# Kernel optimization log

Hardware: AMD Instinct MI355X
Metric: run time of the kernel (lower is better)

Reference implementation:

```python
import jax, jax.numpy as jnp
import numpy as np

T = 1024
H_DIM = 2048
VOCAB = 32000
N_EXPERTS = 8
TOP_K = 2
MOE_I = 1024
SHARED_I = 1024
N_HEADS = 16
Q_LORA = 512
KV_LORA = 256
NOPE = 64
ROPE = 32
V_D = 64
EPS = 1e-6
ROUTED_SCALE = 2.5
NEG = -1e30


def rmsnorm(x, w, eps=EPS):
    return x * jax.lax.rsqrt(jnp.mean(x * x, axis=-1, keepdims=True) + eps) * w


def rope_cos_sin(positions):
    inv_freq = 1.0 / (10000.0 ** (jnp.arange(0, ROPE, 2, dtype=jnp.float32) / ROPE))
    freqs = positions.astype(jnp.float32)[:, None] * inv_freq  # [T, ROPE//2]
    return jnp.cos(freqs), jnp.sin(freqs)


def apply_rope(x, cos, sin):
    # interleaved (non-neox) rotary, as DeepSeek MLA uses
    x1, x2 = x[..., 0::2], x[..., 1::2]
    return jnp.stack([x1 * cos - x2 * sin, x1 * sin + x2 * cos], axis=-1).reshape(x.shape)


def setup_inputs() -> dict:
    key = jax.random.key(0)
    ks = jax.random.split(key, 26)
    s = 0.02

    def w(k, shape, scale=s):
        return jax.random.normal(k, shape, dtype=jnp.float32) * scale

    return {
        'input_ids': jax.random.randint(ks[0], (T,), 0, VOCAB, dtype=jnp.int32),
        'positions': jnp.arange(T, dtype=jnp.int32),
        'previous_hidden_states': jax.random.normal(ks[1], (T, H_DIM), dtype=jnp.float32),
        'embed': w(ks[2], (VOCAB, H_DIM), 1.0),
        'enorm_w': jnp.ones((H_DIM,), jnp.float32),
        'hnorm_w': jnp.ones((H_DIM,), jnp.float32),
        'eh_proj_w': w(ks[3], (2 * H_DIM, H_DIM)),
        'in_ln_w': jnp.ones((H_DIM,), jnp.float32),
        'post_ln_w': jnp.ones((H_DIM,), jnp.float32),
        'q_a_w': w(ks[4], (H_DIM, Q_LORA)),
        'q_a_ln_w': jnp.ones((Q_LORA,), jnp.float32),
        'q_b_w': w(ks[5], (Q_LORA, N_HEADS * (NOPE + ROPE))),
        'kv_a_w': w(ks[6], (H_DIM, KV_LORA + ROPE)),
        'kv_a_ln_w': jnp.ones((KV_LORA,), jnp.float32),
        'kv_b_w': w(ks[7], (KV_LORA, N_HEADS * (NOPE + V_D))),
        'o_w': w(ks[8], (N_HEADS * V_D, H_DIM)),
        'gate_w': w(ks[9], (H_DIM, N_EXPERTS)),
        'gate_bias': w(ks[10], (N_EXPERTS,), 0.01),
        'expert_gate_w': w(ks[11], (N_EXPERTS, H_DIM, MOE_I)),
        'expert_up_w': w(ks[12], (N_EXPERTS, H_DIM, MOE_I)),
        'expert_down_w': w(ks[13], (N_EXPERTS, MOE_I, H_DIM)),
        'shared_gate_w': w(ks[14], (H_DIM, SHARED_I)),
        'shared_up_w': w(ks[15], (H_DIM, SHARED_I)),
        'shared_down_w': w(ks[16], (SHARED_I, H_DIM)),
    }


def reference(input_ids, positions, previous_hidden_states, embed, enorm_w, hnorm_w,
              eh_proj_w, in_ln_w, post_ln_w, q_a_w, q_a_ln_w, q_b_w, kv_a_w, kv_a_ln_w,
              kv_b_w, o_w, gate_w, gate_bias, expert_gate_w, expert_up_w, expert_down_w,
              shared_gate_w, shared_up_w, shared_down_w):
    # --- MTP head: RMSNorm x2 + concat + linear ---
    e = embed[input_ids]                                         # [T, h]
    cat_in = jnp.concatenate([rmsnorm(e, enorm_w),
                              rmsnorm(previous_hidden_states, hnorm_w)], axis=-1)
    x0 = cat_in @ eh_proj_w                                      # [T, h]

    # --- decoder layer: MLA attention ---
    resid = x0
    h = rmsnorm(x0, in_ln_w)
    q_a = rmsnorm(h @ q_a_w, q_a_ln_w)                           # [T, q_lora]
    q = (q_a @ q_b_w).reshape(T, N_HEADS, NOPE + ROPE)
    q_nope, q_pe = q[..., :NOPE], q[..., NOPE:]
    kv_a = h @ kv_a_w                                            # [T, kv_lora+rope]
    kv_c, k_pe = kv_a[:, :KV_LORA], kv_a[:, KV_LORA:]
    kv = (rmsnorm(kv_c, kv_a_ln_w) @ kv_b_w).reshape(T, N_HEADS, NOPE + V_D)
    k_nope, v = kv[..., :NOPE], kv[..., NOPE:]
    cos, sin = rope_cos_sin(positions)                           # [T, ROPE//2]
    q_pe = apply_rope(q_pe, cos[:, None, :], sin[:, None, :])
    k_pe = apply_rope(k_pe, cos, sin)
    qf = jnp.concatenate([q_nope, q_pe], axis=-1)                # [T, H, dq]
    kf = jnp.concatenate([k_nope,
                          jnp.broadcast_to(k_pe[:, None, :], (T, N_HEADS, ROPE))], axis=-1)
    scale = (NOPE + ROPE) ** -0.5
    scores = jnp.einsum('thd,shd->hts', qf, kf) * scale          # [H, T, T]
    causal = positions[:, None] >= positions[None, :]
    scores = jnp.where(causal[None], scores, NEG)
    probs = jax.nn.softmax(scores, axis=-1)
    o = jnp.einsum('hts,shv->thv', probs, v).reshape(T, N_HEADS * V_D)
    attn_out = o @ o_w

    resid = resid + attn_out
    h2 = rmsnorm(resid, post_ln_w)

    # --- DeepSeek-V3 MoE: sigmoid gating + bias-corrected top-k ---
    logits = h2 @ gate_w                                         # [T, E]
    sig = jax.nn.sigmoid(logits)
    _, top_idx = jax.lax.top_k(sig + gate_bias, TOP_K)           # selection uses bias
    top_w = jnp.take_along_axis(sig, top_idx, axis=1)            # weights from raw scores
    top_w = top_w / (jnp.sum(top_w, axis=-1, keepdims=True) + 1e-20)
    combine = (jax.nn.one_hot(top_idx, N_EXPERTS, dtype=h2.dtype)
               * top_w[..., None]).sum(axis=1) * ROUTED_SCALE    # [T, E]
    g = jnp.einsum('th,ehi->tei', h2, expert_gate_w)
    u = jnp.einsum('th,ehi->tei', h2, expert_up_w)
    d = jnp.einsum('tei,eih->teh', jax.nn.silu(g) * u, expert_down_w)
    routed = jnp.einsum('teh,te->th', d, combine)
    shared = (jax.nn.silu(h2 @ shared_gate_w) * (h2 @ shared_up_w)) @ shared_down_w
    mlp_out = routed + shared

    # module returns mtp_hidden + mtp_residual
    return mlp_out + resid
```

## Files before the change

### kernel.cpp

```cpp
#include <hip/hip_runtime.h>
#include <hip/hip_bf16.h>
#include <math.h>

constexpr int T_ = 1024;
constexpr int HDIM = 2048;
constexpr int NH = 16;
constexpr int QKD = 96;
constexpr int VD = 64;
constexpr int MAXTILES = 32;
constexpr float EPSF = 1e-6f;

using f32x4 = __attribute__((ext_vector_type(4))) float;
using s16x8 = __attribute__((ext_vector_type(8))) short;
using s16x4 = __attribute__((ext_vector_type(4))) short;

constexpr size_t OF_CATH  = 0;
constexpr size_t OF_CATL  = 2097152;
constexpr size_t OF_X0    = 4194304;
constexpr size_t OF_MACT  = 6291456;
constexpr size_t OF_HH    = 8388608;
constexpr size_t OF_HL    = 9437184;
constexpr size_t OF_QBUF  = 11010048;
constexpr size_t OF_KVBUF = 12877824;
constexpr size_t OF_QAH   = 14974976;
constexpr size_t OF_QAL   = 15237120;
constexpr size_t OF_KVCNH = 15499264;
constexpr size_t OF_KVCNL = 15630336;
constexpr size_t OF_QFH   = 15761408;
constexpr size_t OF_QFL   = 16547840;
constexpr size_t OF_KFH   = 17334272;
constexpr size_t OF_KFL   = 18120704;
constexpr size_t OF_VBH   = 18907136;
constexpr size_t OF_VBL   = 19431424;
constexpr size_t OF_OBH   = 19955712;
constexpr size_t OF_OBL   = 20480000;
constexpr size_t OF_ATT   = 21004288;
constexpr size_t OF_H2BF  = 23101440;
constexpr size_t OF_ROUT  = 24674304;
constexpr size_t OF_EHTH  = 24682752;
constexpr size_t OF_EHTL  = 28877056;
constexpr size_t OF_QBTH  = 34119936;
constexpr size_t OF_QBTL  = 34513152;
constexpr size_t OF_KVBTH = 35561728;
constexpr size_t OF_KVBTL = 35823872;
constexpr size_t OF_OWTH  = 36086016;
constexpr size_t OF_OWTL  = 37134592;
constexpr size_t OF_MD    = 38183168;
constexpr size_t OF_QKRAW = 44474624;
constexpr size_t OF_BATH  = 45293824;
constexpr size_t OF_BATL  = 46145792;

__device__ __forceinline__ short f2bf(float f) {
    union { float f; unsigned u; } x; x.f = f;
    unsigned r = x.u + 0x7fffu + ((x.u >> 16) & 1u);
    return (short)(r >> 16);
}
__device__ __forceinline__ float bf2f(short h) {
    union { unsigned u; float f; } x; x.u = ((unsigned)(unsigned short)h) << 16; return x.f;
}
__device__ __forceinline__ int swz(int r, int k) {
    return (r << 6) + ((((k >> 3) ^ (r & 7)) << 3) | (k & 7));
}
__device__ __forceinline__ void gload16(const void* g, void* l) {
    __builtin_amdgcn_global_load_lds((__attribute__((address_space(1))) void*)g,
                                     (__attribute__((address_space(3))) void*)l, 16, 0, 0);
}

__device__ __forceinline__ float block_sum(float v) {
    __shared__ float sbuf[9];
    int lane = threadIdx.x & 63;
    int wid  = threadIdx.x >> 6;
#pragma unroll
    for (int off = 32; off > 0; off >>= 1) v += __shfl_down(v, off);
    __syncthreads();
    if (lane == 0) sbuf[wid] = v;
    __syncthreads();
    if (threadIdx.x == 0) {
        float s = 0.f;
        int nw = blockDim.x >> 6;
        for (int i = 0; i < nw; i++) s += sbuf[i];
        sbuf[8] = s;
    }
    __syncthreads();
    return sbuf[8];
}

struct TJobs {
    const float* W[6];
    short* Whi[6];
    short* Wlo[6];
    int K[6];
    int N[6];
    int nbx[6];
    int base[7];
};

__global__ void transpose_multi_kernel(TJobs J) {
    int bid = blockIdx.x;
    int j = 0;
#pragma unroll
    for (int i = 1; i < 6; i++) if (bid >= J.base[i]) j = i;
    int local = bid - J.base[j];
    int K = J.K[j], N = J.N[j];
    int bx = local % J.nbx[j], by = local / J.nbx[j];
    const float* W = J.W[j];
    short* Whi = J.Whi[j];
    short* Wlo = J.Wlo[j];

    __shared__ float tile[64][65];
    int k0 = bx * 64, n0 = by * 64;
    int tn = threadIdx.x & 63;
    int tk4 = threadIdx.x >> 6;
#pragma unroll 4
    for (int i = 0; i < 16; i++) {
        int kk = tk4 * 16 + i;
        int gn = n0 + tn;
        tile[kk][tn] = (gn < N) ? W[(size_t)(k0 + kk) * N + gn] : 0.f;
    }
    __syncthreads();
    int on = threadIdx.x >> 2;
    int oc = threadIdx.x & 3;
#pragma unroll 4
    for (int i = 0; i < 16; i++) {
        int kk = oc * 16 + i;
        float v = tile[kk][on];
        short hh = f2bf(v);
        size_t o = (size_t)(n0 + on) * K + k0 + kk;
        Whi[o] = hh;
        Wlo[o] = f2bf(v - bf2f(hh));
    }
}

__global__ void embed_cat_kernel(const int* __restrict__ ids, const float* __restrict__ embed,
                                 const float* __restrict__ enorm, const float* __restrict__ prev,
                                 const float* __restrict__ hnorm, short* __restrict__ ch,
                                 short* __restrict__ cl) {
    int t = blockIdx.x;
    const float* e = embed + (size_t)ids[t] * HDIM;
    float ss = 0.f;
    for (int i = threadIdx.x; i < HDIM; i += blockDim.x) { float v = e[i]; ss += v * v; }
    float r = rsqrtf(block_sum(ss) / HDIM + EPSF);
    for (int i = threadIdx.x; i < HDIM; i += blockDim.x) {
        float v = e[i] * r * enorm[i];
        short hh = f2bf(v);
        ch[(size_t)t * 4096 + i] = hh;
        cl[(size_t)t * 4096 + i] = f2bf(v - bf2f(hh));
    }
    const float* p = prev + (size_t)t * HDIM;
    ss = 0.f;
    for (int i = threadIdx.x; i < HDIM; i += blockDim.x) { float v = p[i]; ss += v * v; }
    r = rsqrtf(block_sum(ss) / HDIM + EPSF);
    for (int i = threadIdx.x; i < HDIM; i += blockDim.x) {
        float v = p[i] * r * hnorm[i];
        short hh = f2bf(v);
        ch[(size_t)t * 4096 + 2048 + i] = hh;
        cl[(size_t)t * 4096 + 2048 + i] = f2bf(v - bf2f(hh));
    }
}

__global__ void rmsnorm_kernel(const float* __restrict__ in, int in_stride, int width,
                               const float* __restrict__ w, float* __restrict__ outf,
                               short* __restrict__ outh, short* __restrict__ outl, int out_stride) {
    int t = blockIdx.x;
    const float* x = in + (size_t)t * in_stride;
    float ss = 0.f;
    for (int i = threadIdx.x; i < width; i += blockDim.x) { float v = x[i]; ss += v * v; }
    float r = rsqrtf(block_sum(ss) / width + EPSF);
    size_t ob = (size_t)t * out_stride;
    for (int i = threadIdx.x; i < width; i += blockDim.x) {
        float v = x[i] * r * w[i];
        if (outf) outf[ob + i] = v;
        if (outh) {
            short hh = f2bf(v);
            outh[ob + i] = hh;
            if (outl) outl[ob + i] = f2bf(v - bf2f(hh));
        }
    }
}

__global__ void rmsnorm_qkv_kernel(const float* __restrict__ qkraw, const float* __restrict__ wq,
                                   const float* __restrict__ wkv, short* __restrict__ qaH,
                                   short* __restrict__ qaL, short* __restrict__ kvcnH,
                                   short* __restrict__ kvcnL) {
    int t = blockIdx.x;
    const float* row = qkraw + (size_t)t * 800;
    float ss = 0.f;
    for (int i = threadIdx.x; i < 512; i += blockDim.x) { float v = row[i]; ss += v * v; }
    float r = rsqrtf(block_sum(ss) / 512.f + EPSF);
    for (int i = threadIdx.x; i < 512; i += blockDim.x) {
        float v = row[i] * r * wq[i];
        short hh = f2bf(v);
        qaH[(size_t)t * 512 + i] = hh;
        qaL[(size_t)t * 512 + i] = f2bf(v - bf2f(hh));
    }
    ss = 0.f;
    for (int i = threadIdx.x; i < 256; i += blockDim.x) { float v = row[512 + i]; ss += v * v; }
    r = rsqrtf(block_sum(ss) / 256.f + EPSF);
    for (int i = threadIdx.x; i < 256; i += blockDim.x) {
        float v = row[512 + i] * r * wkv[i];
        short hh = f2bf(v);
        kvcnH[(size_t)t * 256 + i] = hh;
        kvcnL[(size_t)t * 256 + i] = f2bf(v - bf2f(hh));
    }
}

template<bool SPLIT>
__global__ __launch_bounds__(256) void gemm_planes(const short* __restrict__ Ahi, const short* __restrict__ Alo,
                                                   const short* __restrict__ Bhi, const short* __restrict__ Blo,
                                                   float* __restrict__ C, int M, int N, int K) {
    __shared__ short As[SPLIT ? 2 : 1][128 * 64];
    __shared__ short Bs[SPLIT ? 2 : 1][64 * 64];
    const int tid = threadIdx.x;
    const int lane = tid & 63, wid = tid >> 6;
    const int g = lane >> 4, li = lane & 15;
    const int wm = wid >> 1, wn = wid & 1;
    const int row0 = blockIdx.y * 128, col0 = blockIdx.x * 64;

    f32x4 acc[4][2];
#pragma unroll
    for (int mi = 0; mi < 4; mi++)
#pragma unroll
        for (int ni = 0; ni < 2; ni++)
#pragma unroll
            for (int r = 0; r < 4; r++) acc[mi][ni][r] = 0.f;

    for (int k0 = 0; k0 < K; k0 += 64) {
#pragma unroll
        for (int j = 0; j < 4; j++) {
            int blkI = wid * 4 + j;
            int cid = blkI * 64 + lane;
            int r = cid >> 3, c = (cid & 7) ^ (r & 7);
            gload16(&Ahi[(size_t)(row0 + r) * K + k0 + c * 8], &As[0][blkI * 512]);
            if constexpr (SPLIT)
                gload16(&Alo[(size_t)(row0 + r) * K + k0 + c * 8], &As[1][blkI * 512]);
        }
#pragma unroll
        for (int j = 0; j < 2; j++) {
            int blkI = wid * 2 + j;
            int cid = blkI * 64 + lane;
            int r = cid >> 3, c = (cid & 7) ^ (r & 7);
            gload16(&Bhi[(size_t)(col0 + r) * K + k0 + c * 8], &Bs[0][blkI * 512]);
            if constexpr (SPLIT)
                gload16(&Blo[(size_t)(col0 + r) * K + k0 + c * 8], &Bs[1][blkI * 512]);
        }
        __syncthreads();
#pragma unroll
        for (int kk = 0; kk < 64; kk += 32) {
            s16x8 ah[4], bh[2];
#pragma unroll
            for (int mi = 0; mi < 4; mi++) ah[mi] = *(const s16x8*)&As[0][swz(wm * 64 + mi * 16 + li, kk + g * 8)];
#pragma unroll
            for (int ni = 0; ni < 2; ni++) bh[ni] = *(const s16x8*)&Bs[0][swz(wn * 32 + ni * 16 + li, kk + g * 8)];
            if constexpr (SPLIT) {
                s16x8 al[4], bl[2];
#pragma unroll
                for (int mi = 0; mi < 4; mi++) al[mi] = *(const s16x8*)&As[1][swz(wm * 64 + mi * 16 + li, kk + g * 8)];
#pragma unroll
                for (int ni = 0; ni < 2; ni++) bl[ni] = *(const s16x8*)&Bs[1][swz(wn * 32 + ni * 16 + li, kk + g * 8)];
#pragma unroll
                for (int mi = 0; mi < 4; mi++)
#pragma unroll
                    for (int ni = 0; ni < 2; ni++) {
                        acc[mi][ni] = __builtin_amdgcn_mfma_f32_16x16x32_bf16(ah[mi], bh[ni], acc[mi][ni], 0, 0, 0);
                        acc[mi][ni] = __builtin_amdgcn_mfma_f32_16x16x32_bf16(al[mi], bh[ni], acc[mi][ni], 0, 0, 0);
                        acc[mi][ni] = __builtin_amdgcn_mfma_f32_16x16x32_bf16(ah[mi], bl[ni], acc[mi][ni], 0, 0, 0);
                    }
            } else {
#pragma unroll
                for (int mi = 0; mi < 4; mi++)
#pragma unroll
                    for (int ni = 0; ni < 2; ni++)
                        acc[mi][ni] = __builtin_amdgcn_mfma_f32_16x16x32_bf16(ah[mi], bh[ni], acc[mi][ni], 0, 0, 0);
            }
        }
        __syncthreads();
    }
#pragma unroll
    for (int mi = 0; mi < 4; mi++)
#pragma unroll
        for (int ni = 0; ni < 2; ni++) {
            int gc = col0 + wn * 32 + ni * 16 + li;
            if (gc < N) {
#pragma unroll
                for (int r = 0; r < 4; r++) {
                    int gr = row0 + wm * 64 + mi * 16 + g * 4 + r;
                    C[(size_t)gr * N + gc] = acc[mi][ni][r];
                }
            }
        }
}

__global__ __launch_bounds__(256) void moe_gateup(const short* __restrict__ h2bf, const int* __restrict__ sorted_t,
                                                  const float* __restrict__ Wg, const float* __restrict__ Wu,
                                                  const float* __restrict__ Sg, const float* __restrict__ Su,
                                                  short* __restrict__ Cact, const int4* __restrict__ tilemap,
                                                  int K, int N) {
    int4 tm = tilemap[blockIdx.y];
    int nrows = tm.z;
    if (nrows == 0) return;
    const float* Bg = (tm.x < 8) ? Wg + (size_t)tm.x * K * N : Sg;
    const float* Bu = (tm.x < 8) ? Wu + (size_t)tm.x * K * N : Su;

    __shared__ short As[128 * 64];
    alignas(16) __shared__ short Bgs[64][72];
    alignas(16) __shared__ short Bus[64][72];
    const int tid = threadIdx.x;
    const int lane = tid & 63, wid = tid >> 6;
    const int g = lane >> 4, li = lane & 15;
    const int wm = wid >> 1, wn = wid & 1;
    const int col0 = blockIdx.x * 64;

    int tokens[4];
#pragma unroll
    for (int j = 0; j < 4; j++) {
        int blkI = wid * 4 + j;
        int cid = blkI * 64 + lane;
        int r = cid >> 3;
        int slot = tm.y + r;
        tokens[j] = (slot < 2048) ? sorted_t[slot] : (slot - 2048);
    }

    f32x4 accg[4][2], accu[4][2];
#pragma unroll
    for (int mi = 0; mi < 4; mi++)
#pragma unroll
        for (int ni = 0; ni < 2; ni++)
#pragma unroll
            for (int r = 0; r < 4; r++) { accg[mi][ni][r] = 0.f; accu[mi][ni][r] = 0.f; }

    const int skb = (tid >> 4) << 2, snb = (tid & 15) << 2;

    for (int k0 = 0; k0 < K; k0 += 64) {
#pragma unroll
        for (int j = 0; j < 4; j++) {
            int blkI = wid * 4 + j;
            int cid = blkI * 64 + lane;
            int r = cid >> 3, c = (cid & 7) ^ (r & 7);
            gload16(&h2bf[(size_t)tokens[j] * K + k0 + c * 8], &As[blkI * 512]);
        }
        {
            float4 rg[4], ru[4];
#pragma unroll
            for (int kk = 0; kk < 4; kk++) {
                rg[kk] = *(const float4*)(Bg + (size_t)(k0 + skb + kk) * N + col0 + snb);
                ru[kk] = *(const float4*)(Bu + (size_t)(k0 + skb + kk) * N + col0 + snb);
            }
#pragma unroll
            for (int n = 0; n < 4; n++) {
                s16x4 wg4, wu4;
                wg4[0] = f2bf((&rg[0].x)[n]); wg4[1] = f2bf((&rg[1].x)[n]);
                wg4[2] = f2bf((&rg[2].x)[n]); wg4[3] = f2bf((&rg[3].x)[n]);
                wu4[0] = f2bf((&ru[0].x)[n]); wu4[1] = f2bf((&ru[1].x)[n]);
                wu4[2] = f2bf((&ru[2].x)[n]); wu4[3] = f2bf((&ru[3].x)[n]);
                *(s16x4*)&Bgs[snb + n][skb] = wg4;
                *(s16x4*)&Bus[snb + n][skb] = wu4;
            }
        }
        __syncthreads();
#pragma unroll
        for (int kk = 0; kk < 64; kk += 32) {
            s16x8 a[4], bg2[2], bu2[2];
#pragma unroll
            for (int mi = 0; mi < 4; mi++) a[mi] = *(const s16x8*)&As[swz(wm * 64 + mi * 16 + li, kk + g * 8)];
#pragma unroll
            for (int ni = 0; ni < 2; ni++) {
                bg2[ni] = *(const s16x8*)&Bgs[wn * 32 + ni * 16 + li][kk + g * 8];
                bu2[ni] = *(const s16x8*)&Bus[wn * 32 + ni * 16 + li][kk + g * 8];
            }
#pragma unroll
            for (int mi = 0; mi < 4; mi++)
#pragma unroll
                for (int ni = 0; ni < 2; ni++) {
                    accg[mi][ni] = __builtin_amdgcn_mfma_f32_16x16x32_bf16(a[mi], bg2[ni], accg[mi][ni], 0, 0, 0);
                    accu[mi][ni] = __builtin_amdgcn_mfma_f32_16x16x32_bf16(a[mi], bu2[ni], accu[mi][ni], 0, 0, 0);
                }
        }
        __syncthreads();
    }
#pragma unroll
    for (int mi = 0; mi < 4; mi++)
#pragma unroll
        for (int ni = 0; ni < 2; ni++) {
            int gc = col0 + wn * 32 + ni * 16 + li;
#pragma unroll
            for (int r = 0; r < 4; r++) {
                int gr = wm * 64 + mi * 16 + g * 4 + r;
                if (gr < nrows) {
                    float x = accg[mi][ni][r], u = accu[mi][ni][r];
                    Cact[(size_t)(tm.y + gr) * N + gc] = f2bf((x / (1.f + expf(-x))) * u);
                }
            }
        }
}

__global__ __launch_bounds__(256) void moe_down(const short* __restrict__ Abase, const float* __restrict__ Wall,
                                                const float* __restrict__ Sd, float* __restrict__ Cbase,
                                                const int4* __restrict__ tilemap, int K, int N) {
    int4 tm = tilemap[blockIdx.y];
    int nrows = tm.z;
    if (nrows == 0) return;
    const short* A = Abase + (size_t)tm.y * K;
    float* C = Cbase + (size_t)tm.y * N;
    const float* B = (tm.x < 8) ? Wall + (size_t)tm.x * K * N : Sd;

    __shared__ short As[128 * 64];
    alignas(16) __shared__ short Bs[64][72];
    const int tid = threadIdx.x;
    const int lane = tid & 63, wid = tid >> 6;
    const int g = lane >> 4, li = lane & 15;
    const int wm = wid >> 1, wn = wid & 1;
    const int col0 = blockIdx.x * 64;

    f32x4 acc[4][2];
#pragma unroll
    for (int mi = 0; mi < 4; mi++)
#pragma unroll
        for (int ni = 0; ni < 2; ni++)
#pragma unroll
            for (int r = 0; r < 4; r++) acc[mi][ni][r] = 0.f;

    const int skb = (tid >> 4) << 2, snb = (tid & 15) << 2;

    for (int k0 = 0; k0 < K; k0 += 64) {
#pragma unroll
        for (int j = 0; j < 4; j++) {
            int blkI = wid * 4 + j;
            int cid = blkI * 64 + lane;
            int r = cid >> 3, c = (cid & 7) ^ (r & 7);
            gload16(&A[(size_t)r * K + k0 + c * 8], &As[blkI * 512]);
        }
        {
            float4 r4[4];
#pragma unroll
            for (int kk = 0; kk < 4; kk++)
                r4[kk] = *(const float4*)(B + (size_t)(k0 + skb + kk) * N + col0 + snb);
#pragma unroll
            for (int n = 0; n < 4; n++) {
                s16x4 w;
                w[0] = f2bf((&r4[0].x)[n]); w[1] = f2bf((&r4[1].x)[n]);
                w[2] = f2bf((&r4[2].x)[n]); w[3] = f2bf((&r4[3].x)[n]);
                *(s16x4*)&Bs[snb + n][skb] = w;
            }
        }
        __syncthreads();
#pragma unroll
        for (int kk = 0; kk < 64; kk += 32) {
            s16x8 a[4], b[2];
#pragma unroll
            for (int mi = 0; mi < 4; mi++) a[mi] = *(const s16x8*)&As[swz(wm * 64 + mi * 16 + li, kk + g * 8)];
#pragma unroll
            for (int ni = 0; ni < 2; ni++) b[ni] = *(const s16x8*)&Bs[wn * 32 + ni * 16 + li][kk + g * 8];
#pragma unroll
            for (int mi = 0; mi < 4; mi++)
#pragma unroll
                for (int ni = 0; ni < 2; ni++)
                    acc[mi][ni] = __builtin_amdgcn_mfma_f32_16x16x32_bf16(a[mi], b[ni], acc[mi][ni], 0, 0, 0);
        }
        __syncthreads();
    }
#pragma unroll
    for (int mi = 0; mi < 4; mi++)
#pragma unroll
        for (int ni = 0; ni < 2; ni++) {
            int gc = col0 + wn * 32 + ni * 16 + li;
#pragma unroll
            for (int r = 0; r < 4; r++) {
                int gr = wm * 64 + mi * 16 + g * 4 + r;
                if (gr < nrows) C[(size_t)gr * N + gc] = acc[mi][ni][r];
            }
        }
}

__global__ void prep_qkv_kernel(const float* __restrict__ q, const float* __restrict__ qkraw,
                                const float* __restrict__ kv, const int* __restrict__ positions,
                                short* __restrict__ qfh, short* __restrict__ qfl,
                                short* __restrict__ kfh, short* __restrict__ kfl,
                                short* __restrict__ vbh, short* __restrict__ vbl) {
    int t = blockIdx.x;
    __shared__ float cs[16], sn[16];
    if (threadIdx.x < 16) {
        float invf = powf(10000.f, -(float)(2 * threadIdx.x) / 32.f);
        float fr = (float)positions[t] * invf;
        cs[threadIdx.x] = cosf(fr);
        sn[threadIdx.x] = sinf(fr);
    }
    __syncthreads();
    for (int i = threadIdx.x; i < NH * QKD; i += blockDim.x) {
        int h = i / QKD, d = i % QKD;
        float val;
        if (d < 64) val = q[(size_t)t * 1536 + h * QKD + d];
        else {
            int r = d - 64, pr = r >> 1;
            float x1 = q[(size_t)t * 1536 + h * QKD + 64 + 2 * pr];
            float x2 = q[(size_t)t * 1536 + h * QKD + 64 + 2 * pr + 1];
            val = (r & 1) ? (x1 * sn[pr] + x2 * cs[pr]) : (x1 * cs[pr] - x2 * sn[pr]);
        }
        short hh = f2bf(val);
        qfh[(size_t)t * 1536 + i] = hh;
        qfl[(size_t)t * 1536 + i] = f2bf(val - bf2f(hh));
    }
    for (int i = threadIdx.x; i < NH * QKD; i += blockDim.x) {
        int h = i / QKD, d = i % QKD;
        float val;
        if (d < 64) val = kv[(size_t)t * 2048 + h * 128 + d];
        else {
            int r = d - 64, pr = r >> 1;
            float x1 = qkraw[(size_t)t * 800 + 768 + 2 * pr];
            float x2 = qkraw[(size_t)t * 800 + 768 + 2 * pr + 1];
            val = (r & 1) ? (x1 * sn[pr] + x2 * cs[pr]) : (x1 * cs[pr] - x2 * sn[pr]);
        }
        short hh = f2bf(val);
        kfh[(size_t)t * 1536 + i] = hh;
        kfl[(size_t)t * 1536 + i] = f2bf(val - bf2f(hh));
    }
    for (int i = threadIdx.x; i < NH * VD; i += blockDim.x) {
        int h = i / VD, d = i % VD;
        float val = kv[(size_t)t * 2048 + h * 128 + 64 + d];
        short hh = f2bf(val);
        vbh[(size_t)t * 1024 + i] = hh;
        vbl[(size_t)t * 1024 + i] = f2bf(val - bf2f(hh));
    }
}

__global__ __launch_bounds__(256) void attn_mfma_kernel(const short* __restrict__ qfh, const short* __restrict__ qfl,
                                                        const short* __restrict__ kfh, const short* __restrict__ kfl,
                                                        const short* __restrict__ vbh, const short* __restrict__ vbl,
                                                        short* __restrict__ obh, short* __restrict__ obl) {
    __shared__ short K_hi[64][104], K_lo[64][104];
    __shared__ short Vt_hi[64][72], Vt_lo[64][72];
    __shared__ short P_hi[4][16][72], P_lo[4][16][72];
    const int qt = blockIdx.x, h = blockIdx.y;
    const int tid = threadIdx.x, lane = tid & 63, w = tid >> 6;
    const int g = lane >> 4, li = lane & 15;

    s16x8 q_hi[3], q_lo[3];
    {
        const short* qb_h = qfh + (size_t)(qt * 64 + w * 16 + li) * 1536 + h * QKD;
        const short* qb_l = qfl + (size_t)(qt * 64 + w * 16 + li) * 1536 + h * QKD;
#pragma unroll
        for (int ks = 0; ks < 3; ks++) {
            q_hi[ks] = *(const s16x8*)(qb_h + ks * 32 + g * 8);
            q_lo[ks] = *(const s16x8*)(qb_l + ks * 32 + g * 8);
        }
    }

    f32x4 acc_o[4];
#pragma unroll
    for (int nc = 0; nc < 4; nc++)
#pragma unroll
        for (int r = 0; r < 4; r++) acc_o[nc][r] = 0.f;
    float m4[4] = {-1e30f, -1e30f, -1e30f, -1e30f};
    float l4[4] = {0.f, 0.f, 0.f, 0.f};
    const float scale = 0.102062072616f;

    for (int kt = 0; kt <= qt; kt++) {
#pragma unroll
        for (int it = 0; it < 3; it++) {
            int cid = it * 256 + tid;
            int key = cid / 12, c = cid % 12;
            *(s16x8*)&K_hi[key][c * 8] = *(const s16x8*)&kfh[(size_t)(kt * 64 + key) * 1536 + h * QKD + c * 8];
            *(s16x8*)&K_lo[key][c * 8] = *(const s16x8*)&kfl[(size_t)(kt * 64 + key) * 1536 + h * QKD + c * 8];
        }
#pragma unroll
        for (int it = 0; it < 2; it++) {
            int cid = it * 256 + tid;
            int key = cid >> 3, vc = cid & 7;
            s16x8 vh = *(const s16x8*)&vbh[(size_t)(kt * 64 + key) * 1024 + h * VD + vc * 8];
            s16x8 vl = *(const s16x8*)&vbl[(size_t)(kt * 64 + key) * 1024 + h * VD + vc * 8];
#pragma unroll
            for (int j = 0; j < 8; j++) {
                Vt_hi[vc * 8 + j][key] = vh[j];
                Vt_lo[vc * 8 + j][key] = vl[j];
            }
        }
        __syncthreads();

        f32x4 acc_s[4];
#pragma unroll
        for (int kc = 0; kc < 4; kc++)
#pragma unroll
            for (int r = 0; r < 4; r++) acc_s[kc][r] = 0.f;
#pragma unroll
        for (int ks = 0; ks < 3; ks++) {
#pragma unroll
            for (int kc = 0; kc < 4; kc++) {
                s16x8 kh = *(const s16x8*)&K_hi[kc * 16 + li][ks * 32 + g * 8];
                s16x8 kl = *(const s16x8*)&K_lo[kc * 16 + li][ks * 32 + g * 8];
                acc_s[kc] = __builtin_amdgcn_mfma_f32_16x16x32_bf16(q_hi[ks], kh, acc_s[kc], 0, 0, 0);
                acc_s[kc] = __builtin_amdgcn_mfma_f32_16x16x32_bf16(q_lo[ks], kh, acc_s[kc], 0, 0, 0);
                acc_s[kc] = __builtin_amdgcn_mfma_f32_16x16x32_bf16(q_hi[ks], kl, acc_s[kc], 0, 0, 0);
            }
        }
#pragma unroll
        for (int kc = 0; kc < 4; kc++)
#pragma unroll
            for (int r = 0; r < 4; r++) acc_s[kc][r] *= scale;
        if (kt == qt) {
#pragma unroll
            for (int kc = 0; kc < 4; kc++) {
                int key = kt * 64 + kc * 16 + li;
#pragma unroll
                for (int r = 0; r < 4; r++) {
                    int qr = qt * 64 + w * 16 + g * 4 + r;
                    if (key > qr) acc_s[kc][r] = -1e30f;
                }
            }
        }
        float tm4[4];
#pragma unroll
        for (int r = 0; r < 4; r++)
            tm4[r] = fmaxf(fmaxf(acc_s[0][r], acc_s[1][r]), fmaxf(acc_s[2][r], acc_s[3][r]));
#pragma unroll
        for (int off = 1; off < 16; off <<= 1)
#pragma unroll
            for (int r = 0; r < 4; r++) tm4[r] = fmaxf(tm4[r], __shfl_xor(tm4[r], off));
        float alpha[4];
#pragma unroll
        for (int r = 0; r < 4; r++) {
            float mn = fmaxf(m4[r], tm4[r]);
            alpha[r] = __expf(m4[r] - mn);
            m4[r] = mn;
        }
        float rs[4] = {0.f, 0.f, 0.f, 0.f};
#pragma unroll
        for (int kc = 0; kc < 4; kc++)
#pragma unroll
            for (int r = 0; r < 4; r++) {
                float p = __expf(acc_s[kc][r] - m4[r]);
                rs[r] += p;
                short hh = f2bf(p);
                P_hi[w][g * 4 + r][kc * 16 + li] = hh;
                P_lo[w][g * 4 + r][kc * 16 + li] = f2bf(p - bf2f(hh));
            }
#pragma unroll
        for (int off = 1; off < 16; off <<= 1)
#pragma unroll
            for (int r = 0; r < 4; r++) rs[r] += __shfl_xor(rs[r], off);
#pragma unroll
        for (int r = 0; r < 4; r++) l4[r] = l4[r] * alpha[r] + rs[r];
#pragma unroll
        for (int nc = 0; nc < 4; nc++)
#pragma unroll
            for (int r = 0; r < 4; r++) acc_o[nc][r] *= alpha[r];
#pragma unroll
        for (int ks = 0; ks < 2; ks++) {
            s16x8 ph = *(const s16x8*)&P_hi[w][li][ks * 32 + g * 8];
            s16x8 pl = *(const s16x8*)&P_lo[w][li][ks * 32 + g * 8];
#pragma unroll
            for (int nc = 0; nc < 4; nc++) {
                s16x8 vh = *(const s16x8*)&Vt_hi[nc * 16 + li][ks * 32 + g * 8];
                s16x8 vl = *(const s16x8*)&Vt_lo[nc * 16 + li][ks * 32 + g * 8];
                acc_o[nc] = __builtin_amdgcn_mfma_f32_16x16x32_bf16(ph, vh, acc_o[nc], 0, 0, 0);
                acc_o[nc] = __builtin_amdgcn_mfma_f32_16x16x32_bf16(pl, vh, acc_o[nc], 0, 0, 0);
                acc_o[nc] = __builtin_amdgcn_mfma_f32_16x16x32_bf16(ph, vl, acc_o[nc], 0, 0, 0);
            }
        }
        __syncthreads();
    }
    float inv[4];
#pragma unroll
    for (int r = 0; r < 4; r++) inv[r] = 1.f / l4[r];
#pragma unroll
    for (int nc = 0; nc < 4; nc++)
#pragma unroll
        for (int r = 0; r < 4; r++) {
            float o = acc_o[nc][r] * inv[r];
            size_t idx = (size_t)(qt * 64 + w * 16 + g * 4 + r) * 1024 + h * VD + nc * 16 + li;
            short hh = f2bf(o);
            obh[idx] = hh;
            obl[idx] = f2bf(o - bf2f(hh));
        }
}

__global__ __launch_bounds__(256) void fused_post_attn(float* __restrict__ x0, const float* __restrict__ att,
                                                       const float* __restrict__ w, const float* __restrict__ gate_w,
                                                       const float* __restrict__ gate_bias,
                                                       short* __restrict__ h2bf, int* __restrict__ topidx,
                                                       float* __restrict__ topw) {
    int t = blockIdx.x;
    float resid[8];
    float ss = 0.f;
#pragma unroll
    for (int j = 0; j < 8; j++) {
        int i = threadIdx.x + j * 256;
        float v = x0[(size_t)t * HDIM + i] + att[(size_t)t * HDIM + i];
        resid[j] = v;
        x0[(size_t)t * HDIM + i] = v;
        ss += v * v;
    }
    float r = rsqrtf(block_sum(ss) / HDIM + EPSF);
    float acc[8] = {0.f, 0.f, 0.f, 0.f, 0.f, 0.f, 0.f, 0.f};
#pragma unroll
    for (int j = 0; j < 8; j++) {
        int i = threadIdx.x + j * 256;
        float v = resid[j] * r * w[i];
        h2bf[(size_t)t * HDIM + i] = f2bf(v);
        const float* gw = gate_w + (size_t)i * 8;
        float4 g0 = *(const float4*)gw;
        float4 g1 = *(const float4*)(gw + 4);
        acc[0] = fmaf(v, g0.x, acc[0]); acc[1] = fmaf(v, g0.y, acc[1]);
        acc[2] = fmaf(v, g0.z, acc[2]); acc[3] = fmaf(v, g0.w, acc[3]);
        acc[4] = fmaf(v, g1.x, acc[4]); acc[5] = fmaf(v, g1.y, acc[5]);
        acc[6] = fmaf(v, g1.z, acc[6]); acc[7] = fmaf(v, g1.w, acc[7]);
    }
    __shared__ float logits[8];
    for (int e = 0; e < 8; e++) {
        float s = block_sum(acc[e]);
        if (threadIdx.x == 0) logits[e] = s;
    }
    __syncthreads();
    if (threadIdx.x == 0) {
        float sig[8], sc[8];
        for (int e = 0; e < 8; e++) {
            sig[e] = 1.f / (1.f + expf(-logits[e]));
            sc[e] = sig[e] + gate_bias[e];
        }
        int i0 = 0;
        for (int e = 1; e < 8; e++) if (sc[e] > sc[i0]) i0 = e;
        int i1 = -1;
        for (int e = 0; e < 8; e++) if (e != i0 && (i1 < 0 || sc[e] > sc[i1])) i1 = e;
        float w0 = sig[i0], w1 = sig[i1], s = w0 + w1 + 1e-20f;
        topidx[t * 2 + 0] = i0; topidx[t * 2 + 1] = i1;
        topw[t * 2 + 0] = w0 / s; topw[t * 2 + 1] = w1 / s;
    }
}

__global__ void sort_kernel(const int* __restrict__ topidx, int* __restrict__ sorted_t,
                            int* __restrict__ slotpos, int4* __restrict__ tilemap) {
    __shared__ int counts[8], offs[9];
    int wid = threadIdx.x >> 6, lane = threadIdx.x & 63;
    int cnt = 0;
    for (int base = 0; base < 2 * T_; base += 64) {
        int e = topidx[base + lane];
        unsigned long long m = __ballot(e == wid);
        cnt += __popcll(m);
    }
    if (lane == 0) counts[wid] = cnt;
    __syncthreads();
    if (threadIdx.x == 0) {
        offs[0] = 0;
        for (int e = 0; e < 8; e++) offs[e + 1] = offs[e] + counts[e];
    }
    __syncthreads();
    int pos = offs[wid];
    for (int base = 0; base < 2 * T_; base += 64) {
        int sl = base + lane;
        int e = topidx[sl];
        bool match = (e == wid);
        unsigned long long m = __ballot(match);
        if (match) {
            int before = __popcll(m & ((1ull << lane) - 1ull));
            int pp = pos + before;
            sorted_t[pp] = sl >> 1;
            slotpos[sl] = pp;
        }
        pos += __popcll(m);
    }
    __syncthreads();
    if (threadIdx.x == 0) {
        int nt = 0;
        for (int e = 0; e < 8; e++) {
            int c = counts[e], o = offs[e];
            for (int r = 0; r < c; r += 128) {
                tilemap[nt] = make_int4(e, o + r, min(128, c - r), 0);
                nt++;
            }
        }
        for (int r = 0; r < 8; r++) {
            tilemap[nt] = make_int4(8, 2048 + r * 128, 128, 0);
            nt++;
        }
        for (int i = nt; i < MAXTILES; i++) tilemap[i] = make_int4(0, 0, 0, 0);
    }
}

__global__ void final_kernel(const float* __restrict__ resid, const float* __restrict__ md,
                             const int* __restrict__ slotpos, const float* __restrict__ topw,
                             float* __restrict__ out) {
    int t = blockIdx.x;
    int p0 = slotpos[t * 2 + 0], p1 = slotpos[t * 2 + 1];
    float w0 = topw[t * 2 + 0] * 2.5f, w1 = topw[t * 2 + 1] * 2.5f;
    const float* mds = md + (size_t)(2048 + t) * HDIM;
    for (int c = threadIdx.x; c < HDIM; c += blockDim.x) {
        float v = resid[(size_t)t * HDIM + c] + mds[c]
                + w0 * md[(size_t)p0 * HDIM + c] + w1 * md[(size_t)p1 * HDIM + c];
        out[(size_t)t * HDIM + c] = v;
    }
}

extern "C" void kernel_launch(void* const* d_in, const int* in_sizes, int n_in,
                              void* d_out, int out_size, void* d_ws, size_t ws_size,
                              hipStream_t stream) {
    (void)in_sizes; (void)n_in; (void)out_size; (void)ws_size;
    const int*   input_ids = (const int*)d_in[0];
    const int*   positions = (const int*)d_in[1];
    const float* prev      = (const float*)d_in[2];
    const float* embed     = (const float*)d_in[3];
    const float* enorm_w   = (const float*)d_in[4];
    const float* hnorm_w   = (const float*)d_in[5];
    const float* eh_proj_w = (const float*)d_in[6];
    const float* in_ln_w   = (const float*)d_in[7];
    const float* post_ln_w = (const float*)d_in[8];
    const float* q_a_w     = (const float*)d_in[9];
    const float* q_a_ln_w  = (const float*)d_in[10];
    const float* q_b_w     = (const float*)d_in[11];
    const float* kv_a_w    = (const float*)d_in[12];
    const float* kv_a_ln_w = (const float*)d_in[13];
    const float* kv_b_w    = (const float*)d_in[14];
    const float* o_w       = (const float*)d_in[15];
    const float* gate_w    = (const float*)d_in[16];
    const float* gate_bias = (const float*)d_in[17];
    const float* exp_g     = (const float*)d_in[18];
    const float* exp_u     = (const float*)d_in[19];
    const float* exp_d     = (const float*)d_in[20];
    const float* sh_g      = (const float*)d_in[21];
    const float* sh_u      = (const float*)d_in[22];
    const float* sh_d      = (const float*)d_in[23];
    float* out = (float*)d_out;

    float* ws = (float*)d_ws;
    short* catH  = (short*)(ws + OF_CATH);
    short* catL  = (short*)(ws + OF_CATL);
    float* x0    = ws + OF_X0;
    short* mact  = (short*)(ws + OF_MACT);
    short* hH    = (short*)(ws + OF_HH);
    short* hL    = (short*)(ws + OF_HL);
    float* qbuf  = ws + OF_QBUF;
    float* kvbuf = ws + OF_KVBUF;
    short* qaH   = (short*)(ws + OF_QAH);
    short* qaL   = (short*)(ws + OF_QAL);
    short* kvcnH = (short*)(ws + OF_KVCNH);
    short* kvcnL = (short*)(ws + OF_KVCNL);
    short* qfH   = (short*)(ws + OF_QFH);
    short* qfL   = (short*)(ws + OF_QFL);
    short* kfH   = (short*)(ws + OF_KFH);
    short* kfL   = (short*)(ws + OF_KFL);
    short* vbH   = (short*)(ws + OF_VBH);
    short* vbL   = (short*)(ws + OF_VBL);
    short* obH   = (short*)(ws + OF_OBH);
    short* obL   = (short*)(ws + OF_OBL);
    float* att   = ws + OF_ATT;
    short* h2bf  = (short*)(ws + OF_H2BF);
    float* md    = ws + OF_MD;
    float* qkraw = ws + OF_QKRAW;
    short* batH  = (short*)(ws + OF_BATH);
    short* batL  = (short*)(ws + OF_BATL);
    int*   ri       = (int*)(ws + OF_ROUT);
    int*   topidx   = ri;
    int*   sorted_t = ri + 2048;
    int*   slotpos  = ri + 4096;
    int4*  tilemap  = (int4*)(ri + 6144);
    float* topw     = (float*)(ri + 6144 + 4 * MAXTILES);
    short* ehTH  = (short*)(ws + OF_EHTH);
    short* ehTL  = (short*)(ws + OF_EHTL);
    short* qbTH  = (short*)(ws + OF_QBTH);
    short* qbTL  = (short*)(ws + OF_QBTL);
    short* kvbTH = (short*)(ws + OF_KVBTH);
    short* kvbTL = (short*)(ws + OF_KVBTL);
    short* owTH  = (short*)(ws + OF_OWTH);
    short* owTL  = (short*)(ws + OF_OWTL);

    dim3 blk(256);

    TJobs J;
    J.W[0] = eh_proj_w; J.Whi[0] = ehTH; J.Wlo[0] = ehTL; J.K[0] = 4096; J.N[0] = 2048; J.nbx[0] = 64;
    J.W[1] = q_a_w; J.Whi[1] = batH; J.Wlo[1] = batL; J.K[1] = 2048; J.N[1] = 512; J.nbx[1] = 32;
    J.W[2] = kv_a_w; J.Whi[2] = batH + (size_t)512 * 2048; J.Wlo[2] = batL + (size_t)512 * 2048;
    J.K[2] = 2048; J.N[2] = 288; J.nbx[2] = 32;
    J.W[3] = q_b_w; J.Whi[3] = qbTH; J.Wlo[3] = qbTL; J.K[3] = 512; J.N[3] = 1536; J.nbx[3] = 8;
    J.W[4] = kv_b_w; J.Whi[4] = kvbTH; J.Wlo[4] = kvbTL; J.K[4] = 256; J.N[4] = 2048; J.nbx[4] = 4;
    J.W[5] = o_w; J.Whi[5] = owTH; J.Wlo[5] = owTL; J.K[5] = 1024; J.N[5] = 2048; J.nbx[5] = 16;
    int nby[6] = {32, 8, 5, 24, 32, 32};
    J.base[0] = 0;
    for (int i = 0; i < 6; i++) J.base[i + 1] = J.base[i] + J.nbx[i] * nby[i];
    transpose_multi_kernel<<<J.base[6], blk, 0, stream>>>(J);

    embed_cat_kernel<<<T_, blk, 0, stream>>>(input_ids, embed, enorm_w, prev, hnorm_w, catH, catL);
    gemm_planes<true><<<dim3(32, 8), blk, 0, stream>>>(catH, catL, ehTH, ehTL, x0, T_, 2048, 4096);
    rmsnorm_kernel<<<T_, blk, 0, stream>>>(x0, 2048, 2048, in_ln_w, nullptr, hH, hL, 2048);
    gemm_planes<true><<<dim3(13, 8), blk, 0, stream>>>(hH, hL, batH, batL, qkraw, T_, 800, 2048);
    rmsnorm_qkv_kernel<<<T_, blk, 0, stream>>>(qkraw, q_a_ln_w, kv_a_ln_w, qaH, qaL, kvcnH, kvcnL);
    gemm_planes<true><<<dim3(24, 8), blk, 0, stream>>>(qaH, qaL, qbTH, qbTL, qbuf, T_, 1536, 512);
    gemm_planes<true><<<dim3(32, 8), blk, 0, stream>>>(kvcnH, kvcnL, kvbTH, kvbTL, kvbuf, T_, 2048, 256);
    prep_qkv_kernel<<<T_, blk, 0, stream>>>(qbuf, qkraw, kvbuf, positions, qfH, qfL, kfH, kfL, vbH, vbL);
    attn_mfma_kernel<<<dim3(T_ / 64, NH), blk, 0, stream>>>(qfH, qfL, kfH, kfL, vbH, vbL, obH, obL);
    gemm_planes<true><<<dim3(32, 8), blk, 0, stream>>>(obH, obL, owTH, owTL, att, T_, 2048, 1024);
    fused_post_attn<<<T_, blk, 0, stream>>>(x0, att, post_ln_w, gate_w, gate_bias, h2bf, topidx, topw);
    sort_kernel<<<1, 512, 0, stream>>>(topidx, sorted_t, slotpos, tilemap);
    moe_gateup<<<dim3(16, MAXTILES), blk, 0, stream>>>(h2bf, sorted_t, exp_g, exp_u, sh_g, sh_u, mact, tilemap, 2048, 1024);
    moe_down<<<dim3(32, MAXTILES), blk, 0, stream>>>(mact, exp_d, sh_d, md, tilemap, 1024, 2048);
    final_kernel<<<T_, blk, 0, stream>>>(x0, md, slotpos, topw, out);
}
```

Baseline: 538.7 us.

## Grow MoE GEMM tiles to 256 rows with 512-thread blocks

Measured after the change: 516.8 us. -4.1%, faster.

```diff
diff --git a/kernel.cpp b/kernel.cpp
--- a/kernel.cpp
+++ b/kernel.cpp
@@ -290,7 +290,7 @@
         }
 }
 
-__global__ __launch_bounds__(256) void moe_gateup(const short* __restrict__ h2bf, const int* __restrict__ sorted_t,
+__global__ __launch_bounds__(512) void moe_gateup(const short* __restrict__ h2bf, const int* __restrict__ sorted_t,
                                                   const float* __restrict__ Wg, const float* __restrict__ Wu,
                                                   const float* __restrict__ Sg, const float* __restrict__ Su,
                                                   short* __restrict__ Cact, const int4* __restrict__ tilemap,
@@ -301,7 +301,7 @@
     const float* Bg = (tm.x < 8) ? Wg + (size_t)tm.x * K * N : Sg;
     const float* Bu = (tm.x < 8) ? Wu + (size_t)tm.x * K * N : Su;
 
-    __shared__ short As[128 * 64];
+    __shared__ short As[256 * 64];
     alignas(16) __shared__ short Bgs[64][72];
     alignas(16) __shared__ short Bus[64][72];
     const int tid = threadIdx.x;
@@ -328,7 +328,8 @@
 #pragma unroll
             for (int r = 0; r < 4; r++) { accg[mi][ni][r] = 0.f; accu[mi][ni][r] = 0.f; }
 
-    const int skb = (tid >> 4) << 2, snb = (tid & 15) << 2;
+    const int t2 = tid & 255;
+    const int skb = (t2 >> 4) << 2, snb = (t2 & 15) << 2;
 
     for (int k0 = 0; k0 < K; k0 += 64) {
 #pragma unroll
@@ -339,21 +340,18 @@
             gload16(&h2bf[(size_t)tokens[j] * K + k0 + c * 8], &As[blkI * 512]);
         }
         {
-            float4 rg[4], ru[4];
-#pragma unroll
-            for (int kk = 0; kk < 4; kk++) {
-                rg[kk] = *(const float4*)(Bg + (size_t)(k0 + skb + kk) * N + col0 + snb);
-                ru[kk] = *(const float4*)(Bu + (size_t)(k0 + skb + kk) * N + col0 + snb);
-            }
+            const float* B = (tid < 256) ? Bg : Bu;
+            short (*Bst)[72] = (tid < 256) ? Bgs : Bus;
+            float4 r4[4];
+#pragma unroll
+            for (int kk = 0; kk < 4; kk++)
+                r4[kk] = *(const float4*)(B + (size_t)(k0 + skb + kk) * N + col0 + snb);
 #pragma unroll
             for (int n = 0; n < 4; n++) {
-                s16x4 wg4, wu4;
-                wg4[0] = f2bf((&rg[0].x)[n]); wg4[1] = f2bf((&rg[1].x)[n]);
-                wg4[2] = f2bf((&rg[2].x)[n]); wg4[3] = f2bf((&rg[3].x)[n]);
-                wu4[0] = f2bf((&ru[0].x)[n]); wu4[1] = f2bf((&ru[1].x)[n]);
-                wu4[2] = f2bf((&ru[2].x)[n]); wu4[3] = f2bf((&ru[3].x)[n]);
-                *(s16x4*)&Bgs[snb + n][skb] = wg4;
-                *(s16x4*)&Bus[snb + n][skb] = wu4;
+                s16x4 w4;
+                w4[0] = f2bf((&r4[0].x)[n]); w4[1] = f2bf((&r4[1].x)[n]);
+                w4[2] = f2bf((&r4[2].x)[n]); w4[3] = f2bf((&r4[3].x)[n]);
+                *(s16x4*)&Bst[snb + n][skb] = w4;
             }
         }
         __syncthreads();
@@ -393,7 +391,7 @@
         }
 }
 
-__global__ __launch_bounds__(256) void moe_down(const short* __restrict__ Abase, const float* __restrict__ Wall,
+__global__ __launch_bounds__(512) void moe_down(const short* __restrict__ Abase, const float* __restrict__ Wall,
                                                 const float* __restrict__ Sd, float* __restrict__ Cbase,
                                                 const int4* __restrict__ tilemap, int K, int N) {
     int4 tm = tilemap[blockIdx.y];
@@ -403,7 +401,7 @@
     float* C = Cbase + (size_t)tm.y * N;
     const float* B = (tm.x < 8) ? Wall + (size_t)tm.x * K * N : Sd;
 
-    __shared__ short As[128 * 64];
+    __shared__ short As[256 * 64];
     alignas(16) __shared__ short Bs[64][72];
     const int tid = threadIdx.x;
     const int lane = tid & 63, wid = tid >> 6;
@@ -429,17 +427,17 @@
             int r = cid >> 3, c = (cid & 7) ^ (r & 7);
             gload16(&A[(size_t)r * K + k0 + c * 8], &As[blkI * 512]);
         }
-        {
+        if (tid < 256) {
             float4 r4[4];
 #pragma unroll
             for (int kk = 0; kk < 4; kk++)
                 r4[kk] = *(const float4*)(B + (size_t)(k0 + skb + kk) * N + col0 + snb);
 #pragma unroll
             for (int n = 0; n < 4; n++) {
-                s16x4 w;
-                w[0] = f2bf((&r4[0].x)[n]); w[1] = f2bf((&r4[1].x)[n]);
-                w[2] = f2bf((&r4[2].x)[n]); w[3] = f2bf((&r4[3].x)[n]);
-                *(s16x4*)&Bs[snb + n][skb] = w;
+                s16x4 w4;
+                w4[0] = f2bf((&r4[0].x)[n]); w4[1] = f2bf((&r4[1].x)[n]);
+                w4[2] = f2bf((&r4[2].x)[n]); w4[3] = f2bf((&r4[3].x)[n]);
+                *(s16x4*)&Bs[snb + n][skb] = w4;
             }
         }
         __syncthreads();
@@ -761,13 +759,13 @@
         int nt = 0;
         for (int e = 0; e < 8; e++) {
             int c = counts[e], o = offs[e];
-            for (int r = 0; r < c; r += 128) {
-                tilemap[nt] = make_int4(e, o + r, min(128, c - r), 0);
+            for (int r = 0; r < c; r += 256) {
+                tilemap[nt] = make_int4(e, o + r, min(256, c - r), 0);
                 nt++;
             }
         }
-        for (int r = 0; r < 8; r++) {
-            tilemap[nt] = make_int4(8, 2048 + r * 128, 128, 0);
+        for (int r = 0; r < 4; r++) {
+            tilemap[nt] = make_int4(8, 2048 + r * 256, 256, 0);
             nt++;
         }
         for (int i = nt; i < MAXTILES; i++) tilemap[i] = make_int4(0, 0, 0, 0);
@@ -887,7 +885,7 @@
     gemm_planes<true><<<dim3(32, 8), blk, 0, stream>>>(obH, obL, owTH, owTL, att, T_, 2048, 1024);
     fused_post_attn<<<T_, blk, 0, stream>>>(x0, att, post_ln_w, gate_w, gate_bias, h2bf, topidx, topw);
     sort_kernel<<<1, 512, 0, stream>>>(topidx, sorted_t, slotpos, tilemap);
-    moe_gateup<<<dim3(16, MAXTILES), blk, 0, stream>>>(h2bf, sorted_t, exp_g, exp_u, sh_g, sh_u, mact, tilemap, 2048, 1024);
-    moe_down<<<dim3(32, MAXTILES), blk, 0, stream>>>(mact, exp_d, sh_d, md, tilemap, 1024, 2048);
+    moe_gateup<<<dim3(16, MAXTILES), dim3(512), 0, stream>>>(h2bf, sorted_t, exp_g, exp_u, sh_g, sh_u, mact, tilemap, 2048, 1024);
+    moe_down<<<dim3(32, MAXTILES), dim3(512), 0, stream>>>(mact, exp_d, sh_d, md, tilemap, 1024, 2048);
     final_kernel<<<T_, blk, 0, stream>>>(x0, md, slotpos, topw, out);
 }
```
